# Performance work log

Hardware: AMD Instinct MI355X
Metric: run time of the kernel (lower is better)

The kernel has to match this reference:

```python
import jax, jax.numpy as jnp
import numpy as np

N_ETA = 7  # number of precip-quantile states / conditional experts
LEV = 34   # vertical levels per prognostic
NPROG = 2  # QT, SLI
H, W_GRID = 512, 1024


def setup_inputs() -> dict:
    key = jax.random.key(0)
    k1, k2, k3, k4, k5 = jax.random.split(key, 5)
    x = jax.random.normal(k1, (NPROG, LEV, H, W_GRID), dtype=jnp.float32)
    Wm = jax.random.normal(k2, (N_ETA, NPROG * LEV, NPROG * LEV), dtype=jnp.float32) * 0.05
    b = jax.random.normal(k3, (N_ETA, NPROG * LEV), dtype=jnp.float32) * 0.05
    # row-stochastic Markov transition matrix over eta states
    Tu = jax.random.uniform(k4, (N_ETA, N_ETA), dtype=jnp.float32) + 0.1
    T = Tu / jnp.sum(Tu, axis=1, keepdims=True)
    eta = jax.random.randint(k5, (H, W_GRID), 0, N_ETA, dtype=jnp.int32)
    return {"x": x, "W": Wm, "b": b, "T": T, "eta": eta}


def reference(x, W, b, T, eta):
    # --- update_eta: per-pixel Markov transition, on-device categorical sampling ---
    # logits[h, w, k] = log T[eta[h, w], k]
    logits = jnp.log(T[eta] + 1e-9)  # [H, W, N_ETA]
    new_eta = jax.random.categorical(jax.random.key(42), logits, axis=-1)  # [H, W] int

    # --- dense compute-all-experts, mask-combine (as in original forward) ---
    nprog, lev, h, w = x.shape
    feat = x.reshape(nprog * lev, h, w)  # [F, H, W], F = 68
    out = jnp.zeros_like(feat)
    for e in range(N_ETA):  # small fixed expert loop
        pred = jnp.einsum('of,fhw->ohw', W[e], feat) + b[e][:, None, None]
        out = jnp.where(new_eta[None, :, :] == e, pred, out)
    return out.reshape(nprog, lev, h, w)
```

## Files before the change

kernel.cpp:

```cpp
#include <hip/hip_runtime.h>
#include <stdint.h>
#include <math.h>

#define HW    524288
#define NETA  7
#define F     68
#define OC    17

#define WSTRIDE 4628
#define WLDS_W  (6 * WSTRIDE + 4624)
#define LDS_TOT (WLDS_W + NETA * F)

__device__ __forceinline__ uint32_t threefry_xor_k42(uint32_t x0, uint32_t x1) {
  const uint32_t ks0 = 0u;
  const uint32_t ks1 = 42u;
  const uint32_t ks2 = 0x1BD11BDAu ^ ks0 ^ ks1;
  x0 += ks0; x1 += ks1;
#define RND(r) { x0 += x1; x1 = (x1 << (r)) | (x1 >> (32 - (r))); x1 ^= x0; }
  RND(13) RND(15) RND(26) RND(6)   x0 += ks1; x1 += ks2 + 1u;
  RND(17) RND(29) RND(16) RND(24)  x0 += ks2; x1 += ks0 + 2u;
  RND(13) RND(15) RND(26) RND(6)   x0 += ks0; x1 += ks1 + 3u;
  RND(17) RND(29) RND(16) RND(24)  x0 += ks1; x1 += ks2 + 4u;
  RND(13) RND(15) RND(26) RND(6)   x0 += ks2; x1 += ks0 + 5u;
#undef RND
  return x0 ^ x1;
}

__global__ void __launch_bounds__(256) eta_kernel(const float* __restrict__ T,
                                                  const int* __restrict__ eta,
                                                  int* __restrict__ eta_new) {
  __shared__ float  rinv32[NETA * NETA];
  __shared__ double rinv64[NETA * NETA];
  const int tid = threadIdx.x;
  if (tid < NETA * NETA) {
    double d = 1.0 / ((double)T[tid] + 1e-9);
    rinv64[tid] = d;
    rinv32[tid] = (float)d;
  }
  __syncthreads();

  const int p = blockIdx.x * 256 + tid;
  const int r = eta[p];

  float w[NETA];
#pragma unroll
  for (int k = 0; k < NETA; k++) {
    const uint32_t bits = threefry_xor_k42(0u, (uint32_t)(7 * p + k));
    const float f = __uint_as_float((bits >> 9) | 0x3f800000u) - 1.0f;
    const float u = (f == 0.0f) ? 1.1754943508222875e-38f : f;
    w[k] = (-__log2f(u)) * rinv32[r * NETA + k];
  }
  float w1 = w[0], w2 = 3.4e38f;
  int e = 0;
#pragma unroll
  for (int k = 1; k < NETA; k++) {
    if (w[k] < w1)      { w2 = w1; w1 = w[k]; e = k; }
    else if (w[k] < w2) { w2 = w[k]; }
  }
  if (!((w2 - w1) > 3e-5f * w2)) {
    double b1 = 1e300;
    e = 0;
    for (int k = 0; k < NETA; k++) {
      const uint32_t bits = threefry_xor_k42(0u, (uint32_t)(7 * p + k));
      const float f = __uint_as_float((bits >> 9) | 0x3f800000u) - 1.0f;
      const double u = (f == 0.0f) ? (double)1.1754943508222875e-38f : (double)f;
      const double wv = -log(u) * rinv64[r * NETA + k];
      if (wv < b1) { b1 = wv; e = k; }
    }
  }
  eta_new[p] = e;
}

__global__ void __launch_bounds__(256, 1) expert_kernel(const float* __restrict__ x,
                                                        const float* __restrict__ W,
                                                        const float* __restrict__ b,
                                                        const int* __restrict__ eta_new,
                                                        float* __restrict__ out) {
  __shared__ __align__(16) float wlds[LDS_TOT];
  const int tid = threadIdx.x;

#pragma unroll
  for (int e = 0; e < NETA; e++) {
    const float* __restrict__ src = W + (size_t)e * (F * F);
    float* dst = wlds + e * WSTRIDE;
    for (int i = tid; i < (F * F) / 4; i += 256) {
      *reinterpret_cast<float4*>(dst + 4 * i) =
          *reinterpret_cast<const float4*>(src + 4 * i);
    }
  }
  for (int i = tid; i < NETA * F; i += 256) wlds[WLDS_W + i] = b[i];
  __syncthreads();

  const int pl = tid & 63;
  const int c  = tid >> 6;

  for (int tile = blockIdx.x; tile < HW / 64; tile += gridDim.x) {
    const int p = tile * 64 + pl;
    const int e = eta_new[p];

    float xv[F];
#pragma unroll
    for (int f = 0; f < F; f++) xv[f] = x[(size_t)f * HW + p];

    const float* wp = wlds + e * WSTRIDE + (c * OC) * F;

    float acc[OC];
#pragma unroll
    for (int o = 0; o < OC; o++) acc[o] = 0.0f;

#pragma unroll
    for (int f4 = 0; f4 < F / 4; f4++) {
      const float x0 = xv[4 * f4 + 0];
      const float x1 = xv[4 * f4 + 1];
      const float x2 = xv[4 * f4 + 2];
      const float x3 = xv[4 * f4 + 3];
#pragma unroll
      for (int o = 0; o < OC; o++) {
        const float4 w = *reinterpret_cast<const float4*>(wp + o * F + 4 * f4);
        float a = acc[o];
        a = fmaf(w.x, x0, a);
        a = fmaf(w.y, x1, a);
        a = fmaf(w.z, x2, a);
        a = fmaf(w.w, x3, a);
        acc[o] = a;
      }
    }

#pragma unroll
    for (int o = 0; o < OC; o++)
      out[(size_t)(c * OC + o) * HW + p] = acc[o] + wlds[WLDS_W + e * F + c * OC + o];
  }
}

extern "C" void kernel_launch(void* const* d_in, const int* in_sizes, int n_in,
                              void* d_out, int out_size, void* d_ws, size_t ws_size,
                              hipStream_t stream) {
  const float* x   = (const float*)d_in[0];
  const float* W   = (const float*)d_in[1];
  const float* b   = (const float*)d_in[2];
  const float* T   = (const float*)d_in[3];
  const int*   eta = (const int*)d_in[4];
  float* out = (float*)d_out;

  int* etabuf = (ws_size >= sizeof(int) * (size_t)HW)
                    ? (int*)d_ws
                    : ((int*)d_out) + (size_t)(F - 1) * HW;

  eta_kernel<<<HW / 256, 256, 0, stream>>>(T, eta, etabuf);
  expert_kernel<<<1024, 256, 0, stream>>>(x, W, b, etabuf, out);
}
```

Measured before the change: 438.5 us.

## Bucket pixels by sampled expert so each wavefront applies one uniform weight matrix

Expert sampling now also counts pixels per expert with wave-level ballots and atomics. A new scatter pass builds a permutation that groups pixel indices by expert. The expert kernel walks this permutation, so each wavefront mostly sees a single expert and reads its weights with uniform loads. This replaces per-lane divergent LDS weight reads in the old kernel. In exchange it adds a memset, an extra kernel, and gathered x loads plus scattered output stores at roughly one-in-seven pixel density. The old path is kept as a fallback when the workspace is too small.

```diff
diff --git a/kernel.cpp b/kernel.cpp
--- a/kernel.cpp
+++ b/kernel.cpp
@@ -6,10 +6,6 @@
 #define NETA  7
 #define F     68
 #define OC    17
-
-#define WSTRIDE 4628
-#define WLDS_W  (6 * WSTRIDE + 4624)
-#define LDS_TOT (WLDS_W + NETA * F)
 
 __device__ __forceinline__ uint32_t threefry_xor_k42(uint32_t x0, uint32_t x1) {
   const uint32_t ks0 = 0u;
@@ -26,22 +22,9 @@
   return x0 ^ x1;
 }
 
-__global__ void __launch_bounds__(256) eta_kernel(const float* __restrict__ T,
-                                                  const int* __restrict__ eta,
-                                                  int* __restrict__ eta_new) {
-  __shared__ float  rinv32[NETA * NETA];
-  __shared__ double rinv64[NETA * NETA];
-  const int tid = threadIdx.x;
-  if (tid < NETA * NETA) {
-    double d = 1.0 / ((double)T[tid] + 1e-9);
-    rinv64[tid] = d;
-    rinv32[tid] = (float)d;
-  }
-  __syncthreads();
-
-  const int p = blockIdx.x * 256 + tid;
-  const int r = eta[p];
-
+__device__ __forceinline__ int sample_eta(int p, int r,
+                                          const float* rinv32,
+                                          const double* rinv64) {
   float w[NETA];
 #pragma unroll
   for (int k = 0; k < NETA; k++) {
@@ -68,46 +51,173 @@
       if (wv < b1) { b1 = wv; e = k; }
     }
   }
+  return e;
+}
+
+__global__ void __launch_bounds__(256) eta_count_kernel(const float* __restrict__ T,
+                                                        const int* __restrict__ eta,
+                                                        int* __restrict__ eta_new,
+                                                        int* __restrict__ counts) {
+  __shared__ float  rinv32[NETA * NETA];
+  __shared__ double rinv64[NETA * NETA];
+  const int tid = threadIdx.x;
+  if (tid < NETA * NETA) {
+    double d = 1.0 / ((double)T[tid] + 1e-9);
+    rinv64[tid] = d;
+    rinv32[tid] = (float)d;
+  }
+  __syncthreads();
+
+  const int p = blockIdx.x * 256 + tid;
+  const int e = sample_eta(p, eta[p], rinv32, rinv64);
   eta_new[p] = e;
-}
-
-__global__ void __launch_bounds__(256, 1) expert_kernel(const float* __restrict__ x,
-                                                        const float* __restrict__ W,
-                                                        const float* __restrict__ b,
-                                                        const int* __restrict__ eta_new,
-                                                        float* __restrict__ out) {
+
+  const int lane = tid & 63;
+#pragma unroll
+  for (int k = 0; k < NETA; k++) {
+    const unsigned long long m = __ballot(e == k);
+    if (m && lane == (__ffsll(m) - 1))
+      atomicAdd(&counts[k], (int)__popcll(m));
+  }
+}
+
+__global__ void __launch_bounds__(256) scatter_kernel(const int* __restrict__ eta_new,
+                                                      const int* __restrict__ counts,
+                                                      int* __restrict__ cursors,
+                                                      int* __restrict__ perm) {
+  const int lane = threadIdx.x & 63;
+  const int wid  = (blockIdx.x * 256 + threadIdx.x) >> 6;
+
+  int myE[16];
+#pragma unroll
+  for (int j = 0; j < 16; j++)
+    myE[j] = eta_new[wid * 1024 + j * 64 + lane];
+
+  int base_e[NETA];
+  {
+    int a = 0;
+#pragma unroll
+    for (int k = 0; k < NETA; k++) { base_e[k] = a; a += counts[k]; }
+  }
+
+#pragma unroll 1
+  for (int e = 0; e < NETA; e++) {
+    int pre[16];
+    int total = 0;
+#pragma unroll
+    for (int j = 0; j < 16; j++) {
+      pre[j] = total;
+      total += (int)__popcll(__ballot(myE[j] == e));
+    }
+    int wbase = 0;
+    if (lane == 0) wbase = atomicAdd(&cursors[e], total);
+    wbase = __shfl(wbase, 0) + base_e[e];
+#pragma unroll
+    for (int j = 0; j < 16; j++) {
+      const unsigned long long m = __ballot(myE[j] == e);
+      if (myE[j] == e) {
+        const int rank = (int)__popcll(m & ((1ull << lane) - 1));
+        perm[wbase + pre[j] + rank] = (e << 19) | (wid * 1024 + j * 64 + lane);
+      }
+    }
+  }
+}
+
+__global__ void __launch_bounds__(256, 4) expert_bucket_kernel(const float* __restrict__ x,
+                                                               const float* __restrict__ W,
+                                                               const float* __restrict__ b,
+                                                               const int* __restrict__ perm,
+                                                               float* __restrict__ out) {
+  const int s  = blockIdx.x * 256 + threadIdx.x;
+  const int pk = perm[s];
+  const int p  = pk & (HW - 1);
+  const int e  = pk >> 19;
+
+  bool rem = true;
+  while (__any(rem)) {
+    const unsigned long long mm = __ballot(rem);
+    const int lead = __ffsll(mm) - 1;
+    const int e0   = __builtin_amdgcn_readfirstlane(__shfl(e, lead));
+    const bool go  = rem && (e == e0);
+    if (go) {
+      float xv[F];
+#pragma unroll
+      for (int f = 0; f < F; f++) xv[f] = x[(size_t)f * HW + p];
+
+      const float* __restrict__ wb = W + (size_t)e0 * (F * F);
+      const float* __restrict__ bb = b + e0 * F;
+
+#pragma unroll 1
+      for (int og = 0; og < F; og += 4) {
+        float a0 = 0.0f, a1 = 0.0f, a2 = 0.0f, a3 = 0.0f;
+#pragma unroll
+        for (int f = 0; f < F; f++) {
+          const float xf = xv[f];
+          a0 = fmaf(wb[(size_t)(og + 0) * F + f], xf, a0);
+          a1 = fmaf(wb[(size_t)(og + 1) * F + f], xf, a1);
+          a2 = fmaf(wb[(size_t)(og + 2) * F + f], xf, a2);
+          a3 = fmaf(wb[(size_t)(og + 3) * F + f], xf, a3);
+        }
+        out[(size_t)(og + 0) * HW + p] = a0 + bb[og + 0];
+        out[(size_t)(og + 1) * HW + p] = a1 + bb[og + 1];
+        out[(size_t)(og + 2) * HW + p] = a2 + bb[og + 2];
+        out[(size_t)(og + 3) * HW + p] = a3 + bb[og + 3];
+      }
+    }
+    rem = rem && !go;
+  }
+}
+
+#define WSTRIDE 4628
+#define WLDS_W  (6 * WSTRIDE + 4624)
+#define LDS_TOT (WLDS_W + NETA * F)
+
+__global__ void __launch_bounds__(256) eta_kernel_fb(const float* __restrict__ T,
+                                                     const int* __restrict__ eta,
+                                                     int* __restrict__ eta_new) {
+  __shared__ float  rinv32[NETA * NETA];
+  __shared__ double rinv64[NETA * NETA];
+  const int tid = threadIdx.x;
+  if (tid < NETA * NETA) {
+    double d = 1.0 / ((double)T[tid] + 1e-9);
+    rinv64[tid] = d;
+    rinv32[tid] = (float)d;
+  }
+  __syncthreads();
+  const int p = blockIdx.x * 256 + tid;
+  eta_new[p] = sample_eta(p, eta[p], rinv32, rinv64);
+}
+
+__global__ void __launch_bounds__(256, 1) expert_kernel_fb(const float* __restrict__ x,
+                                                           const float* __restrict__ W,
+                                                           const float* __restrict__ b,
+                                                           const int* __restrict__ eta_new,
+                                                           float* __restrict__ out) {
   __shared__ __align__(16) float wlds[LDS_TOT];
   const int tid = threadIdx.x;
-
 #pragma unroll
   for (int e = 0; e < NETA; e++) {
     const float* __restrict__ src = W + (size_t)e * (F * F);
     float* dst = wlds + e * WSTRIDE;
-    for (int i = tid; i < (F * F) / 4; i += 256) {
+    for (int i = tid; i < (F * F) / 4; i += 256)
       *reinterpret_cast<float4*>(dst + 4 * i) =
           *reinterpret_cast<const float4*>(src + 4 * i);
-    }
   }
   for (int i = tid; i < NETA * F; i += 256) wlds[WLDS_W + i] = b[i];
   __syncthreads();
 
   const int pl = tid & 63;
   const int c  = tid >> 6;
-
   for (int tile = blockIdx.x; tile < HW / 64; tile += gridDim.x) {
     const int p = tile * 64 + pl;
     const int e = eta_new[p];
-
     float xv[F];
 #pragma unroll
     for (int f = 0; f < F; f++) xv[f] = x[(size_t)f * HW + p];
-
     const float* wp = wlds + e * WSTRIDE + (c * OC) * F;
-
     float acc[OC];
 #pragma unroll
     for (int o = 0; o < OC; o++) acc[o] = 0.0f;
-
 #pragma unroll
     for (int f4 = 0; f4 < F / 4; f4++) {
       const float x0 = xv[4 * f4 + 0];
@@ -125,7 +235,6 @@
         acc[o] = a;
       }
     }
-
 #pragma unroll
     for (int o = 0; o < OC; o++)
       out[(size_t)(c * OC + o) * HW + p] = acc[o] + wlds[WLDS_W + e * F + c * OC + o];
@@ -142,10 +251,21 @@
   const int*   eta = (const int*)d_in[4];
   float* out = (float*)d_out;
 
-  int* etabuf = (ws_size >= sizeof(int) * (size_t)HW)
-                    ? (int*)d_ws
-                    : ((int*)d_out) + (size_t)(F - 1) * HW;
-
-  eta_kernel<<<HW / 256, 256, 0, stream>>>(T, eta, etabuf);
-  expert_kernel<<<1024, 256, 0, stream>>>(x, W, b, etabuf, out);
-}
+  const size_t need = 16 * sizeof(int) + 2 * (size_t)HW * sizeof(int);
+  if (ws_size >= need) {
+    int* counts  = (int*)d_ws;
+    int* cursors = counts + 8;
+    int* eta_new = counts + 16;
+    int* perm    = eta_new + HW;
+    hipMemsetAsync(counts, 0, 16 * sizeof(int), stream);
+    eta_count_kernel<<<HW / 256, 256, 0, stream>>>(T, eta, eta_new, counts);
+    scatter_kernel<<<HW / 1024 / 4, 256, 0, stream>>>(eta_new, counts, cursors, perm);
+    expert_bucket_kernel<<<HW / 256, 256, 0, stream>>>(x, W, b, perm, out);
+  } else {
+    int* etabuf = (ws_size >= sizeof(int) * (size_t)HW)
+                      ? (int*)d_ws
+                      : ((int*)d_out) + (size_t)(F - 1) * HW;
+    eta_kernel_fb<<<HW / 256, 256, 0, stream>>>(T, eta, etabuf);
+    expert_kernel_fb<<<1024, 256, 0, stream>>>(x, W, b, etabuf, out);
+  }
+}
```

Measured after the change: 1.496 ms. 3.41x slower.
